# Kernel optimization log

Measured on AMD Instinct MI355X. Metric: run time of the kernel, lower is better.

The kernel has to match this reference:

```python
import jax, jax.numpy as jnp
import numpy as np

B, C, H, W = 2, 512, 48, 48
HEADS = 8          # head_dim = C // HEADS = 64
GROUPS = 32        # min(32, ceil(512/4)) = 32
EPS = 1e-5


def setup_inputs() -> dict:
    key = jax.random.key(0)
    ks = jax.random.split(key, 5)
    return {
        "x": jax.random.normal(ks[0], (B, C, H, W), jnp.float32),
        "gn_w": jnp.ones((C,), jnp.float32),
        "gn_b": jnp.zeros((C,), jnp.float32),
        # 1x1 convs stored as [out, in] matrices
        "qkv_w": jax.random.normal(ks[1], (3 * C, C), jnp.float32) / np.float32(np.sqrt(C)),
        "qkv_b": jax.random.normal(ks[2], (3 * C,), jnp.float32) * 0.01,
        "proj_w": jax.random.normal(ks[3], (C, C), jnp.float32) / np.float32(np.sqrt(C)),
        "proj_b": jax.random.normal(ks[4], (C,), jnp.float32) * 0.01,
    }


def _group_norm(x, w, b):
    b_, c_, h_, w_ = x.shape
    xg = x.reshape(b_, GROUPS, c_ // GROUPS, h_, w_)
    mean = xg.mean(axis=(2, 3, 4), keepdims=True)
    var = xg.var(axis=(2, 3, 4), keepdims=True)  # biased, matches F.group_norm
    xn = ((xg - mean) * jax.lax.rsqrt(var + EPS)).reshape(b_, c_, h_, w_)
    return xn * w[None, :, None, None] + b[None, :, None, None]


def reference(x, gn_w, gn_b, qkv_w, qkv_b, proj_w, proj_b):
    bx, cx, hx, wx = x.shape
    d = cx // HEADS
    n = hx * wx
    xn = _group_norm(x, gn_w, gn_b)
    # qkv 1x1 conv -> [B, 3C, H, W]
    y = jnp.einsum('oc,bchw->bohw', qkv_w, xn) + qkv_b[None, :, None, None]
    # torch: y.reshape(B*heads, d, 3, N).unbind(2)  (channel layout: head, chan, qkv)
    qkv = y.reshape(bx * HEADS, d, 3, n)
    q, k, v = qkv[:, :, 0, :], qkv[:, :, 1, :], qkv[:, :, 2, :]
    scale = np.float32(1.0 / np.sqrt(d))
    # AttentionOp: fp32 QK^T + softmax over keys (axis=2)
    w_attn = jax.nn.softmax(jnp.einsum('ncq,nck->nqk', q, k * scale), axis=2)
    a = jnp.einsum('nqk,nck->ncq', w_attn, v).reshape(bx, cx, hx, wx)
    out = jnp.einsum('oc,bchw->bohw', proj_w, a) + proj_b[None, :, None, None]
    return out + x
```

## Files before the change

kernel.cpp:

```cpp
#include <hip/hip_runtime.h>

typedef __bf16 bf16;
typedef __bf16 bf16x8 __attribute__((ext_vector_type(8)));
typedef __bf16 bf16x4 __attribute__((ext_vector_type(4)));
typedef float f32x4 __attribute__((ext_vector_type(4)));

#define B_ 2
#define C_ 512
#define HW_ 2304
#define GROUPS_ 32
#define CPG_ 16
#define EPS_ 1e-5f
#define THR_ 8.0f
#define LOG2E_ 1.44269504f
#define EXP2(x) __builtin_amdgcn_exp2f(x)

__device__ __forceinline__ void gload_lds16(const bf16* g, bf16* l) {
  __builtin_amdgcn_global_load_lds((const __attribute__((address_space(1))) void*)g,
                                   (__attribute__((address_space(3))) void*)l, 16, 0, 0);
}

__global__ __launch_bounds__(256) void pre_k(const float* __restrict__ x,
                                             const float* __restrict__ qkv_w,
                                             const float* __restrict__ qkv_b,
                                             const float* __restrict__ proj_w,
                                             float* __restrict__ ps,
                                             float* __restrict__ pss,
                                             bf16* __restrict__ wqkv,
                                             bf16* __restrict__ wp,
                                             float* __restrict__ bqkv) {
  int blk = blockIdx.x;
  if (blk < 512) {
    int bg = blk >> 3, seg = blk & 7;
    const int n4 = CPG_ * HW_ / 4 / 8;
    const float4* p = (const float4*)(x + (long)bg * CPG_ * HW_) + (long)seg * n4;
    float s = 0.f, ss = 0.f;
    for (int i = threadIdx.x; i < n4; i += 256) {
      float4 v = p[i];
      s += v.x + v.y + v.z + v.w;
      ss += v.x * v.x + v.y * v.y + v.z * v.z + v.w * v.w;
    }
#pragma unroll
    for (int d = 1; d < 64; d <<= 1) { s += __shfl_xor(s, d); ss += __shfl_xor(ss, d); }
    __shared__ float rs[4], rss[4];
    int wave = threadIdx.x >> 6, lane = threadIdx.x & 63;
    if (lane == 0) { rs[wave] = s; rss[wave] = ss; }
    __syncthreads();
    if (threadIdx.x == 0) {
      ps[blk] = rs[0] + rs[1] + rs[2] + rs[3];
      pss[blk] = rss[0] + rss[1] + rss[2] + rss[3];
    }
  } else {
    int idx = (blk - 512) * 256 + threadIdx.x;
    int r = idx >> 9, c = idx & 511;
    int src = (r < 512) ? 3 * r : (r < 1024 ? 3 * (r - 512) + 1 : 3 * (r - 1024) + 2);
    float sc = (r < 512) ? 0.125f * LOG2E_ : 1.0f;
    wqkv[idx] = (bf16)(qkv_w[(long)src * 512 + c] * sc);
    if (idx < 512 * 512) wp[idx] = (bf16)(proj_w[idx]);
    if (idx < 1536) {
      int sb = (idx < 512) ? 3 * idx : (idx < 1024 ? 3 * (idx - 512) + 1 : 3 * (idx - 1024) + 2);
      float sc2 = (idx < 512) ? 0.125f * LOG2E_ : 1.0f;
      bqkv[idx] = qkv_b[sb] * sc2;
    }
  }
}

__global__ __launch_bounds__(256) void gn_apply_k(const float* __restrict__ x,
                                                  const float* __restrict__ gw,
                                                  const float* __restrict__ gb,
                                                  const float* __restrict__ ps,
                                                  const float* __restrict__ pss,
                                                  bf16* __restrict__ xnT) {
  int n0 = blockIdx.x * 64, c0 = blockIdx.y * 32, b = blockIdx.z;
  int nn = n0 + (threadIdx.x & 63);
  int cb = c0 + ((threadIdx.x >> 6) << 3);
  int gi = b * GROUPS_ + (cb >> 4);
  float s = 0.f, ss = 0.f;
#pragma unroll
  for (int k = 0; k < 8; ++k) { s += ps[gi * 8 + k]; ss += pss[gi * 8 + k]; }
  const float invN = 1.0f / (float)(CPG_ * HW_);
  float mu = s * invN;
  float var = ss * invN - mu * mu;
  float rstd = rsqrtf(var + EPS_);
  bf16x8 o;
#pragma unroll
  for (int j = 0; j < 8; ++j) {
    int c = cb + j;
    float sc = rstd * gw[c];
    float sh = gb[c] - mu * sc;
    float v = x[((long)b * C_ + c) * HW_ + nn];
    o[j] = (bf16)(v * sc + sh);
  }
  *(bf16x8*)&xnT[((long)b * HW_ + nn) * C_ + cb] = o;
}

__global__ __launch_bounds__(256) void gemm_qkv_k(const bf16* __restrict__ A,
                                                  const bf16* __restrict__ BT,
                                                  const float* __restrict__ bias,
                                                  bf16* __restrict__ yT,
                                                  bf16* __restrict__ vOut) {
  constexpr int KK = 512;
  constexpr int NSTEP = KK >> 6;
  int b = blockIdx.z;
  A += (long)HW_ * 512 * b;
  yT += (long)HW_ * 1024 * b;
  vOut += (long)512 * HW_ * b;
  int m0 = blockIdx.y * 64, n0 = blockIdx.x * 64;
  int tid = threadIdx.x, lane = tid & 63, wave = tid >> 6;
  int wm = (wave >> 1) << 5, wn = (wave & 1) << 5;
  int fr = lane & 15, g = lane >> 4;
  __shared__ __align__(16) bf16 As[3][64 * 64];
  __shared__ __align__(16) bf16 Bs[3][64 * 64];
  int sr = tid >> 3;
  int swz = (((tid & 7) + sr) & 7) << 3;
  const bf16* gA = A + (long)(m0 + sr) * KK + swz;
  const bf16* gB = BT + (long)(n0 + sr) * KK + swz;
  int o0 = ((g - fr) & 7) << 3;
  int o1 = ((4 + g - fr) & 7) << 3;
  f32x4 acc[2][2] = {};
  gload_lds16(gA, &As[0][tid * 8]);
  gload_lds16(gA + 32 * KK, &As[0][2048 + tid * 8]);
  gload_lds16(gB, &Bs[0][tid * 8]);
  gload_lds16(gB + 32 * KK, &Bs[0][2048 + tid * 8]);
  gload_lds16(gA + 64, &As[1][tid * 8]);
  gload_lds16(gA + 32 * KK + 64, &As[1][2048 + tid * 8]);
  gload_lds16(gB + 64, &Bs[1][tid * 8]);
  gload_lds16(gB + 32 * KK + 64, &Bs[1][2048 + tid * 8]);
  asm volatile("s_waitcnt vmcnt(4)" ::: "memory");
  __builtin_amdgcn_s_barrier();
#pragma unroll
  for (int t = 0; t < NSTEP; ++t) {
    const int cur = t % 3;
    if (t + 2 < NSTEP) {
      const int nb = (t + 2) % 3;
      int k0 = (t + 2) << 6;
      gload_lds16(gA + k0, &As[nb][tid * 8]);
      gload_lds16(gA + 32 * KK + k0, &As[nb][2048 + tid * 8]);
      gload_lds16(gB + k0, &Bs[nb][tid * 8]);
      gload_lds16(gB + 32 * KK + k0, &Bs[nb][2048 + tid * 8]);
    }
    bf16x8 a00 = *(bf16x8*)&As[cur][(wm + fr) * 64 + o0];
    bf16x8 a01 = *(bf16x8*)&As[cur][(wm + fr) * 64 + o1];
    bf16x8 a10 = *(bf16x8*)&As[cur][(wm + 16 + fr) * 64 + o0];
    bf16x8 a11 = *(bf16x8*)&As[cur][(wm + 16 + fr) * 64 + o1];
    bf16x8 b00 = *(bf16x8*)&Bs[cur][(wn + fr) * 64 + o0];
    bf16x8 b01 = *(bf16x8*)&Bs[cur][(wn + fr) * 64 + o1];
    bf16x8 b10 = *(bf16x8*)&Bs[cur][(wn + 16 + fr) * 64 + o0];
    bf16x8 b11 = *(bf16x8*)&Bs[cur][(wn + 16 + fr) * 64 + o1];
    acc[0][0] = __builtin_amdgcn_mfma_f32_16x16x32_bf16(a00, b00, acc[0][0], 0, 0, 0);
    acc[0][0] = __builtin_amdgcn_mfma_f32_16x16x32_bf16(a01, b01, acc[0][0], 0, 0, 0);
    acc[0][1] = __builtin_amdgcn_mfma_f32_16x16x32_bf16(a00, b10, acc[0][1], 0, 0, 0);
    acc[0][1] = __builtin_amdgcn_mfma_f32_16x16x32_bf16(a01, b11, acc[0][1], 0, 0, 0);
    acc[1][0] = __builtin_amdgcn_mfma_f32_16x16x32_bf16(a10, b00, acc[1][0], 0, 0, 0);
    acc[1][0] = __builtin_amdgcn_mfma_f32_16x16x32_bf16(a11, b01, acc[1][0], 0, 0, 0);
    acc[1][1] = __builtin_amdgcn_mfma_f32_16x16x32_bf16(a10, b10, acc[1][1], 0, 0, 0);
    acc[1][1] = __builtin_amdgcn_mfma_f32_16x16x32_bf16(a11, b11, acc[1][1], 0, 0, 0);
    if (t + 2 < NSTEP) {
      asm volatile("s_waitcnt vmcnt(4) lgkmcnt(0)" ::: "memory");
    } else if (t + 1 < NSTEP) {
      asm volatile("s_waitcnt vmcnt(0) lgkmcnt(0)" ::: "memory");
    }
    if (t + 1 < NSTEP) __builtin_amdgcn_s_barrier();
  }
  int rbase = (lane >> 4) << 2;
  if (n0 < 1024) {
#pragma unroll
    for (int mi = 0; mi < 2; ++mi)
#pragma unroll
      for (int nj = 0; nj < 2; ++nj)
#pragma unroll
        for (int reg = 0; reg < 4; ++reg) {
          int row = m0 + wm + (mi << 4) + rbase + reg;
          int col = n0 + wn + (nj << 4) + fr;
          yT[(long)row * 1024 + col] = (bf16)(acc[mi][nj][reg] + bias[col]);
        }
  } else {
#pragma unroll
    for (int mi = 0; mi < 2; ++mi)
#pragma unroll
      for (int nj = 0; nj < 2; ++nj) {
        int row0 = m0 + wm + (mi << 4) + rbase;
        int ch = n0 - 1024 + wn + (nj << 4) + fr;
        float bs = bias[n0 + wn + (nj << 4) + fr];
        bf16x4 ov = {(bf16)(acc[mi][nj][0] + bs), (bf16)(acc[mi][nj][1] + bs),
                     (bf16)(acc[mi][nj][2] + bs), (bf16)(acc[mi][nj][3] + bs)};
        *(bf16x4*)&vOut[(long)ch * HW_ + row0] = ov;
      }
  }
}

template <int BIAS_MODE, bool RESID, typename OUT_T>
__global__ __launch_bounds__(256) void gemm_k(const bf16* __restrict__ A,
                                              const bf16* __restrict__ BT,
                                              const float* __restrict__ bias,
                                              const float* __restrict__ resid,
                                              OUT_T* __restrict__ Cc,
                                              int M, int N,
                                              long sA, long sBT, long sC) {
  constexpr int KK = 512;
  constexpr int NSTEP = KK >> 6;
  int b = blockIdx.z;
  A += sA * b;
  BT += sBT * b;
  Cc += sC * b;
  const float* R = RESID ? (resid + sC * b) : nullptr;
  int m0 = blockIdx.y * 64, n0 = blockIdx.x * 64;
  int tid = threadIdx.x, lane = tid & 63, wave = tid >> 6;
  int wm = (wave >> 1) << 5, wn = (wave & 1) << 5;
  int fr = lane & 15, g = lane >> 4;
  __shared__ __align__(16) bf16 As[3][64 * 64];
  __shared__ __align__(16) bf16 Bs[3][64 * 64];
  int sr = tid >> 3;
  int swz = (((tid & 7) + sr) & 7) << 3;
  const bf16* gA = A + (long)(m0 + sr) * KK + swz;
  const bf16* gB = BT + (long)(n0 + sr) * KK + swz;
  int o0 = ((g - fr) & 7) << 3;
  int o1 = ((4 + g - fr) & 7) << 3;
  f32x4 acc[2][2] = {};
  gload_lds16(gA, &As[0][tid * 8]);
  gload_lds16(gA + 32 * KK, &As[0][2048 + tid * 8]);
  gload_lds16(gB, &Bs[0][tid * 8]);
  gload_lds16(gB + 32 * KK, &Bs[0][2048 + tid * 8]);
  gload_lds16(gA + 64, &As[1][tid * 8]);
  gload_lds16(gA + 32 * KK + 64, &As[1][2048 + tid * 8]);
  gload_lds16(gB + 64, &Bs[1][tid * 8]);
  gload_lds16(gB + 32 * KK + 64, &Bs[1][2048 + tid * 8]);
  asm volatile("s_waitcnt vmcnt(4)" ::: "memory");
  __builtin_amdgcn_s_barrier();
#pragma unroll
  for (int t = 0; t < NSTEP; ++t) {
    const int cur = t % 3;
    if (t + 2 < NSTEP) {
      const int nb = (t + 2) % 3;
      int k0 = (t + 2) << 6;
      gload_lds16(gA + k0, &As[nb][tid * 8]);
      gload_lds16(gA + 32 * KK + k0, &As[nb][2048 + tid * 8]);
      gload_lds16(gB + k0, &Bs[nb][tid * 8]);
      gload_lds16(gB + 32 * KK + k0, &Bs[nb][2048 + tid * 8]);
    }
    bf16x8 a00 = *(bf16x8*)&As[cur][(wm + fr) * 64 + o0];
    bf16x8 a01 = *(bf16x8*)&As[cur][(wm + fr) * 64 + o1];
    bf16x8 a10 = *(bf16x8*)&As[cur][(wm + 16 + fr) * 64 + o0];
    bf16x8 a11 = *(bf16x8*)&As[cur][(wm + 16 + fr) * 64 + o1];
    bf16x8 b00 = *(bf16x8*)&Bs[cur][(wn + fr) * 64 + o0];
    bf16x8 b01 = *(bf16x8*)&Bs[cur][(wn + fr) * 64 + o1];
    bf16x8 b10 = *(bf16x8*)&Bs[cur][(wn + 16 + fr) * 64 + o0];
    bf16x8 b11 = *(bf16x8*)&Bs[cur][(wn + 16 + fr) * 64 + o1];
    acc[0][0] = __builtin_amdgcn_mfma_f32_16x16x32_bf16(a00, b00, acc[0][0], 0, 0, 0);
    acc[0][0] = __builtin_amdgcn_mfma_f32_16x16x32_bf16(a01, b01, acc[0][0], 0, 0, 0);
    acc[0][1] = __builtin_amdgcn_mfma_f32_16x16x32_bf16(a00, b10, acc[0][1], 0, 0, 0);
    acc[0][1] = __builtin_amdgcn_mfma_f32_16x16x32_bf16(a01, b11, acc[0][1], 0, 0, 0);
    acc[1][0] = __builtin_amdgcn_mfma_f32_16x16x32_bf16(a10, b00, acc[1][0], 0, 0, 0);
    acc[1][0] = __builtin_amdgcn_mfma_f32_16x16x32_bf16(a11, b01, acc[1][0], 0, 0, 0);
    acc[1][1] = __builtin_amdgcn_mfma_f32_16x16x32_bf16(a10, b10, acc[1][1], 0, 0, 0);
    acc[1][1] = __builtin_amdgcn_mfma_f32_16x16x32_bf16(a11, b11, acc[1][1], 0, 0, 0);
    if (t + 2 < NSTEP) {
      asm volatile("s_waitcnt vmcnt(4) lgkmcnt(0)" ::: "memory");
    } else if (t + 1 < NSTEP) {
      asm volatile("s_waitcnt vmcnt(0) lgkmcnt(0)" ::: "memory");
    }
    if (t + 1 < NSTEP) __builtin_amdgcn_s_barrier();
  }
  int rbase = (lane >> 4) << 2;
#pragma unroll
  for (int mi = 0; mi < 2; ++mi)
#pragma unroll
    for (int nj = 0; nj < 2; ++nj)
#pragma unroll
      for (int reg = 0; reg < 4; ++reg) {
        int row = m0 + wm + (mi << 4) + rbase + reg;
        int col = n0 + wn + (nj << 4) + fr;
        float v = acc[mi][nj][reg];
        if (BIAS_MODE == 1) v += bias[row];
        if (BIAS_MODE == 2) v += bias[col];
        if (RESID) v += R[(long)row * N + col];
        Cc[(long)row * N + col] = (OUT_T)v;
      }
}

template <int NS>
__global__ __launch_bounds__(512) void attn_k(const bf16* __restrict__ yT,
                                              const bf16* __restrict__ V,
                                              bf16* __restrict__ Op,
                                              float* __restrict__ Mp,
                                              float* __restrict__ Lp) {
  const int n = HW_;
  constexpr int NT = (HW_ / NS) / 64;
  int bh = blockIdx.y, b = bh >> 3, h = bh & 7;
  int split = blockIdx.z;
  int q0 = blockIdx.x * 128;
  int kbeg = split * (n / NS);
  int tid = threadIdx.x, lane = tid & 63, wave = tid >> 6;
  int fr = lane & 15, g = lane >> 4, kg = g << 3;
  const bf16* yTb = yT + (long)b * n * 1024;
  const bf16* Vb = V + ((long)b * C_ + h * 64) * n;
  const bf16* Kb = yTb + 512 + h * 64;

  int qrow = q0 + (wave << 4) + fr;
  const bf16* qp = yTb + (long)qrow * 1024 + h * 64;
  bf16x8 qf0 = *(const bf16x8*)(qp + kg);
  bf16x8 qf1 = *(const bf16x8*)(qp + 32 + kg);

  __shared__ __align__(16) bf16 Kt[2][64][64];
  __shared__ __align__(16) bf16 Vt[2][64][64];

  int o0 = ((g + fr) & 7) << 3;
  int o1 = ((4 + g + fr) & 7) << 3;

  float m_run = -1e30f, l_run = 0.f;
  f32x4 oacc[4] = {};

  int r0 = tid >> 3;
  int ck = tid & 7;
  int c0e = ck << 3;
  int pk = ((ck + r0) & 7) << 3;
  int vs = (c0e & 32) | ((c0e & 8) << 1) | ((c0e & 16) >> 2);
  int cv = vs >> 3, sub = vs & 7;
  int pv0 = (((cv + r0) & 7) << 3) + sub;
  int pv1 = (((cv + 1 + r0) & 7) << 3) + sub;

  const bf16* kptr = Kb + (long)(kbeg + r0) * 1024 + c0e;
  const bf16* vptr = Vb + (long)r0 * n + kbeg + c0e;
  uint4 rk = *(const uint4*)kptr;
  uint4 rv = *(const uint4*)vptr;
  *(uint4*)&Kt[0][r0][pk] = rk;
  *(uint2*)&Vt[0][r0][pv0] = make_uint2(rv.x, rv.y);
  *(uint2*)&Vt[0][r0][pv1] = make_uint2(rv.z, rv.w);
  kptr += 64 * 1024;
  vptr += 64;
  rk = *(const uint4*)kptr;
  rv = *(const uint4*)vptr;
  __syncthreads();

  for (int t = 0; t < NT; ++t) {
    int cur = t & 1;
    f32x4 s[4] = {};
    __builtin_amdgcn_s_setprio(1);
#pragma unroll
    for (int nj = 0; nj < 4; ++nj) {
      bf16x8 kf0 = *(bf16x8*)&Kt[cur][(nj << 4) + fr][o0];
      bf16x8 kf1 = *(bf16x8*)&Kt[cur][(nj << 4) + fr][o1];
      s[nj] = __builtin_amdgcn_mfma_f32_16x16x32_bf16(kf0, qf0, s[nj], 0, 0, 0);
      s[nj] = __builtin_amdgcn_mfma_f32_16x16x32_bf16(kf1, qf1, s[nj], 0, 0, 0);
    }
    __builtin_amdgcn_s_setprio(0);
    if (t + 1 < NT) {
      int nb = cur ^ 1;
      *(uint4*)&Kt[nb][r0][pk] = rk;
      *(uint2*)&Vt[nb][r0][pv0] = make_uint2(rv.x, rv.y);
      *(uint2*)&Vt[nb][r0][pv1] = make_uint2(rv.z, rv.w);
      if (t + 2 < NT) {
        kptr += 64 * 1024;
        vptr += 64;
        rk = *(const uint4*)kptr;
        rv = *(const uint4*)vptr;
      }
    }
    float pm = fmaxf(fmaxf(s[0][0], s[0][1]), fmaxf(s[0][2], s[0][3]));
#pragma unroll
    for (int nj = 1; nj < 4; ++nj)
      pm = fmaxf(pm, fmaxf(fmaxf(s[nj][0], s[nj][1]), fmaxf(s[nj][2], s[nj][3])));
    pm = fmaxf(pm, __shfl_xor(pm, 16));
    pm = fmaxf(pm, __shfl_xor(pm, 32));
    if (__any(pm > m_run + THR_)) {
      float mn = fmaxf(m_run, pm);
      float corr = EXP2(m_run - mn);
      m_run = mn;
      l_run *= corr;
#pragma unroll
      for (int dj = 0; dj < 4; ++dj)
#pragma unroll
        for (int r = 0; r < 4; ++r) oacc[dj][r] *= corr;
    }
    float ls = 0.f;
    bf16x8 pa0, pa1;
#pragma unroll
    for (int r = 0; r < 4; ++r) {
      float p0 = EXP2(s[0][r] - m_run);
      float p1 = EXP2(s[1][r] - m_run);
      float p2 = EXP2(s[2][r] - m_run);
      float p3 = EXP2(s[3][r] - m_run);
      ls += (p0 + p1) + (p2 + p3);
      pa0[r] = (bf16)p0;
      pa0[4 + r] = (bf16)p1;
      pa1[r] = (bf16)p2;
      pa1[4 + r] = (bf16)p3;
    }
    ls += __shfl_xor(ls, 16);
    ls += __shfl_xor(ls, 32);
    l_run += ls;
    __builtin_amdgcn_s_setprio(1);
#pragma unroll
    for (int dj = 0; dj < 4; ++dj) {
      bf16x8 vf0 = *(bf16x8*)&Vt[cur][(dj << 4) + fr][o0];
      bf16x8 vf1 = *(bf16x8*)&Vt[cur][(dj << 4) + fr][o1];
      oacc[dj] = __builtin_amdgcn_mfma_f32_16x16x32_bf16(vf0, pa0, oacc[dj], 0, 0, 0);
      oacc[dj] = __builtin_amdgcn_mfma_f32_16x16x32_bf16(vf1, pa1, oacc[dj], 0, 0, 0);
    }
    __builtin_amdgcn_s_setprio(0);
    __syncthreads();
  }
  long orow = (long)(split * 16 + bh) * n + q0 + (wave << 4) + fr;
#pragma unroll
  for (int dj = 0; dj < 4; ++dj) {
    bf16x4 ov = {(bf16)oacc[dj][0], (bf16)oacc[dj][1], (bf16)oacc[dj][2], (bf16)oacc[dj][3]};
    *(bf16x4*)&Op[orow * 64 + (dj << 4) + (g << 2)] = ov;
  }
  if (g == 0) {
    Mp[orow] = m_run;
    Lp[orow] = l_run;
  }
}

template <int NS>
__global__ __launch_bounds__(256) void attn_merge_k(const bf16* __restrict__ Op,
                                                    const float* __restrict__ Mp,
                                                    const float* __restrict__ Lp,
                                                    bf16* __restrict__ aT) {
  int bh = blockIdx.y, b = bh >> 3, h = bh & 7;
  int gi = blockIdx.x * 256 + threadIdx.x;
  int nrow = gi >> 3, dd8 = (gi & 7) << 3;
  long idx[NS];
  float mm = -1e30f;
#pragma unroll
  for (int s = 0; s < NS; ++s) {
    idx[s] = (long)(s * 16 + bh) * HW_ + nrow;
    mm = fmaxf(mm, Mp[idx[s]]);
  }
  float l = 0.f, w[NS];
#pragma unroll
  for (int s = 0; s < NS; ++s) {
    w[s] = EXP2(Mp[idx[s]] - mm);
    l += Lp[idx[s]] * w[s];
  }
  float invl = 1.f / l;
  float oaccf[8] = {};
#pragma unroll
  for (int s = 0; s < NS; ++s) {
    bf16x8 o = *(const bf16x8*)&Op[idx[s] * 64 + dd8];
    float ws = w[s] * invl;
#pragma unroll
    for (int j = 0; j < 8; ++j) oaccf[j] += (float)o[j] * ws;
  }
  bf16x8 o;
#pragma unroll
  for (int j = 0; j < 8; ++j) o[j] = (bf16)oaccf[j];
  *(bf16x8*)&aT[((long)b * HW_ + nrow) * C_ + h * 64 + dd8] = o;
}

extern "C" void kernel_launch(void* const* d_in, const int* in_sizes, int n_in,
                              void* d_out, int out_size, void* d_ws, size_t ws_size,
                              hipStream_t stream) {
  const float* x = (const float*)d_in[0];
  const float* gn_w = (const float*)d_in[1];
  const float* gn_b = (const float*)d_in[2];
  const float* qkv_w = (const float*)d_in[3];
  const float* qkv_b = (const float*)d_in[4];
  const float* proj_w = (const float*)d_in[5];
  const float* proj_b = (const float*)d_in[6];
  float* out = (float*)d_out;

  char* ws = (char*)d_ws;
  float* ps = (float*)ws;    ws += 2048;
  float* pss = (float*)ws;   ws += 2048;
  float* bqkv = (float*)ws;  ws += 6144;
  bf16* wqkv = (bf16*)ws;    ws += 1536l * 512 * 2;
  bf16* wp = (bf16*)ws;      ws += 512l * 512 * 2;
  bf16* xnT = (bf16*)ws;     ws += 2l * HW_ * 512 * 2;
  bf16* yT = (bf16*)ws;      ws += 2l * HW_ * 1024 * 2;
  bf16* v = (bf16*)ws;       ws += 2l * 512 * HW_ * 2;
  bf16* aT = (bf16*)ws;      ws += 2l * HW_ * 512 * 2;
  bf16* Op = (bf16*)ws;
  size_t base_used = (size_t)(ws - (char*)d_ws);
  size_t need4 = base_used + 4ull * 16 * HW_ * 64 * 2 + 2ull * 4 * 16 * HW_ * 4;
  int NS = (ws_size >= need4) ? 4 : 2;
  ws += (size_t)NS * 16 * HW_ * 64 * 2;
  float* Mp = (float*)ws;    ws += (size_t)NS * 16 * HW_ * 4;
  float* Lp = (float*)ws;    ws += (size_t)NS * 16 * HW_ * 4;

  pre_k<<<3584, 256, 0, stream>>>(x, qkv_w, qkv_b, proj_w, ps, pss, wqkv, wp, bqkv);
  gn_apply_k<<<dim3(36, 16, 2), 256, 0, stream>>>(x, gn_w, gn_b, ps, pss, xnT);
  gemm_qkv_k<<<dim3(24, 36, 2), 256, 0, stream>>>(xnT, wqkv, bqkv, yT, v);
  if (NS == 4) {
    attn_k<4><<<dim3(18, 16, 4), 512, 0, stream>>>(yT, v, Op, Mp, Lp);
    attn_merge_k<4><<<dim3(72, 16), 256, 0, stream>>>(Op, Mp, Lp, aT);
  } else {
    attn_k<2><<<dim3(18, 16, 2), 512, 0, stream>>>(yT, v, Op, Mp, Lp);
    attn_merge_k<2><<<dim3(72, 16), 256, 0, stream>>>(Op, Mp, Lp, aT);
  }
  gemm_k<1, true, float><<<dim3(36, 8, 2), 256, 0, stream>>>(
      wp, aT, proj_b, x, out, 512, 2304, 0, (long)HW_ * 512, 512l * HW_);
}
```

Measured before the change: 85.49 us.

## Fuse split-K attention merge into projection GEMM B-operand load

The separate attention merge kernel, which combined partial softmax outputs into aT, is removed. The projection GEMM now reads the partial outputs plus their max and sum stats, merges them in registers for each K-step, and writes the merged bf16 tile into LDS as the B operand. This drops one launch and the aT round trip through global memory. The cost is that every M-tile block (8 per column) recomputes the merge and rereads the partials, and each step now waits on vmcnt(0) with register-staged loads instead of asynchronous LDS loads. Separately, the group-norm apply kernel computes mean and rstd once per group in shared memory instead of in every thread.

New measurement: 91.60 us. 1.07x slower.

```diff
diff --git a/kernel.cpp b/kernel.cpp
--- a/kernel.cpp
+++ b/kernel.cpp
@@ -74,14 +74,21 @@
   int n0 = blockIdx.x * 64, c0 = blockIdx.y * 32, b = blockIdx.z;
   int nn = n0 + (threadIdx.x & 63);
   int cb = c0 + ((threadIdx.x >> 6) << 3);
-  int gi = b * GROUPS_ + (cb >> 4);
-  float s = 0.f, ss = 0.f;
-#pragma unroll
-  for (int k = 0; k < 8; ++k) { s += ps[gi * 8 + k]; ss += pss[gi * 8 + k]; }
-  const float invN = 1.0f / (float)(CPG_ * HW_);
-  float mu = s * invN;
-  float var = ss * invN - mu * mu;
-  float rstd = rsqrtf(var + EPS_);
+  __shared__ float smu[2], srstd[2];
+  if (threadIdx.x < 2) {
+    int gi = b * GROUPS_ + (c0 >> 4) + threadIdx.x;
+    float s = 0.f, ss = 0.f;
+#pragma unroll
+    for (int k = 0; k < 8; ++k) { s += ps[gi * 8 + k]; ss += pss[gi * 8 + k]; }
+    const float invN = 1.0f / (float)(CPG_ * HW_);
+    float mu = s * invN;
+    float var = ss * invN - mu * mu;
+    smu[threadIdx.x] = mu;
+    srstd[threadIdx.x] = rsqrtf(var + EPS_);
+  }
+  __syncthreads();
+  int gsel = threadIdx.x >> 7;
+  float mu = smu[gsel], rstd = srstd[gsel];
   bf16x8 o;
 #pragma unroll
   for (int j = 0; j < 8; ++j) {
@@ -189,95 +196,6 @@
   }
 }
 
-template <int BIAS_MODE, bool RESID, typename OUT_T>
-__global__ __launch_bounds__(256) void gemm_k(const bf16* __restrict__ A,
-                                              const bf16* __restrict__ BT,
-                                              const float* __restrict__ bias,
-                                              const float* __restrict__ resid,
-                                              OUT_T* __restrict__ Cc,
-                                              int M, int N,
-                                              long sA, long sBT, long sC) {
-  constexpr int KK = 512;
-  constexpr int NSTEP = KK >> 6;
-  int b = blockIdx.z;
-  A += sA * b;
-  BT += sBT * b;
-  Cc += sC * b;
-  const float* R = RESID ? (resid + sC * b) : nullptr;
-  int m0 = blockIdx.y * 64, n0 = blockIdx.x * 64;
-  int tid = threadIdx.x, lane = tid & 63, wave = tid >> 6;
-  int wm = (wave >> 1) << 5, wn = (wave & 1) << 5;
-  int fr = lane & 15, g = lane >> 4;
-  __shared__ __align__(16) bf16 As[3][64 * 64];
-  __shared__ __align__(16) bf16 Bs[3][64 * 64];
-  int sr = tid >> 3;
-  int swz = (((tid & 7) + sr) & 7) << 3;
-  const bf16* gA = A + (long)(m0 + sr) * KK + swz;
-  const bf16* gB = BT + (long)(n0 + sr) * KK + swz;
-  int o0 = ((g - fr) & 7) << 3;
-  int o1 = ((4 + g - fr) & 7) << 3;
-  f32x4 acc[2][2] = {};
-  gload_lds16(gA, &As[0][tid * 8]);
-  gload_lds16(gA + 32 * KK, &As[0][2048 + tid * 8]);
-  gload_lds16(gB, &Bs[0][tid * 8]);
-  gload_lds16(gB + 32 * KK, &Bs[0][2048 + tid * 8]);
-  gload_lds16(gA + 64, &As[1][tid * 8]);
-  gload_lds16(gA + 32 * KK + 64, &As[1][2048 + tid * 8]);
-  gload_lds16(gB + 64, &Bs[1][tid * 8]);
-  gload_lds16(gB + 32 * KK + 64, &Bs[1][2048 + tid * 8]);
-  asm volatile("s_waitcnt vmcnt(4)" ::: "memory");
-  __builtin_amdgcn_s_barrier();
-#pragma unroll
-  for (int t = 0; t < NSTEP; ++t) {
-    const int cur = t % 3;
-    if (t + 2 < NSTEP) {
-      const int nb = (t + 2) % 3;
-      int k0 = (t + 2) << 6;
-      gload_lds16(gA + k0, &As[nb][tid * 8]);
-      gload_lds16(gA + 32 * KK + k0, &As[nb][2048 + tid * 8]);
-      gload_lds16(gB + k0, &Bs[nb][tid * 8]);
-      gload_lds16(gB + 32 * KK + k0, &Bs[nb][2048 + tid * 8]);
-    }
-    bf16x8 a00 = *(bf16x8*)&As[cur][(wm + fr) * 64 + o0];
-    bf16x8 a01 = *(bf16x8*)&As[cur][(wm + fr) * 64 + o1];
-    bf16x8 a10 = *(bf16x8*)&As[cur][(wm + 16 + fr) * 64 + o0];
-    bf16x8 a11 = *(bf16x8*)&As[cur][(wm + 16 + fr) * 64 + o1];
-    bf16x8 b00 = *(bf16x8*)&Bs[cur][(wn + fr) * 64 + o0];
-    bf16x8 b01 = *(bf16x8*)&Bs[cur][(wn + fr) * 64 + o1];
-    bf16x8 b10 = *(bf16x8*)&Bs[cur][(wn + 16 + fr) * 64 + o0];
-    bf16x8 b11 = *(bf16x8*)&Bs[cur][(wn + 16 + fr) * 64 + o1];
-    acc[0][0] = __builtin_amdgcn_mfma_f32_16x16x32_bf16(a00, b00, acc[0][0], 0, 0, 0);
-    acc[0][0] = __builtin_amdgcn_mfma_f32_16x16x32_bf16(a01, b01, acc[0][0], 0, 0, 0);
-    acc[0][1] = __builtin_amdgcn_mfma_f32_16x16x32_bf16(a00, b10, acc[0][1], 0, 0, 0);
-    acc[0][1] = __builtin_amdgcn_mfma_f32_16x16x32_bf16(a01, b11, acc[0][1], 0, 0, 0);
-    acc[1][0] = __builtin_amdgcn_mfma_f32_16x16x32_bf16(a10, b00, acc[1][0], 0, 0, 0);
-    acc[1][0] = __builtin_amdgcn_mfma_f32_16x16x32_bf16(a11, b01, acc[1][0], 0, 0, 0);
-    acc[1][1] = __builtin_amdgcn_mfma_f32_16x16x32_bf16(a10, b10, acc[1][1], 0, 0, 0);
-    acc[1][1] = __builtin_amdgcn_mfma_f32_16x16x32_bf16(a11, b11, acc[1][1], 0, 0, 0);
-    if (t + 2 < NSTEP) {
-      asm volatile("s_waitcnt vmcnt(4) lgkmcnt(0)" ::: "memory");
-    } else if (t + 1 < NSTEP) {
-      asm volatile("s_waitcnt vmcnt(0) lgkmcnt(0)" ::: "memory");
-    }
-    if (t + 1 < NSTEP) __builtin_amdgcn_s_barrier();
-  }
-  int rbase = (lane >> 4) << 2;
-#pragma unroll
-  for (int mi = 0; mi < 2; ++mi)
-#pragma unroll
-    for (int nj = 0; nj < 2; ++nj)
-#pragma unroll
-      for (int reg = 0; reg < 4; ++reg) {
-        int row = m0 + wm + (mi << 4) + rbase + reg;
-        int col = n0 + wn + (nj << 4) + fr;
-        float v = acc[mi][nj][reg];
-        if (BIAS_MODE == 1) v += bias[row];
-        if (BIAS_MODE == 2) v += bias[col];
-        if (RESID) v += R[(long)row * N + col];
-        Cc[(long)row * N + col] = (OUT_T)v;
-      }
-}
-
 template <int NS>
 __global__ __launch_bounds__(512) void attn_k(const bf16* __restrict__ yT,
                                               const bf16* __restrict__ V,
@@ -413,39 +331,126 @@
 }
 
 template <int NS>
-__global__ __launch_bounds__(256) void attn_merge_k(const bf16* __restrict__ Op,
-                                                    const float* __restrict__ Mp,
-                                                    const float* __restrict__ Lp,
-                                                    bf16* __restrict__ aT) {
-  int bh = blockIdx.y, b = bh >> 3, h = bh & 7;
-  int gi = blockIdx.x * 256 + threadIdx.x;
-  int nrow = gi >> 3, dd8 = (gi & 7) << 3;
-  long idx[NS];
-  float mm = -1e30f;
-#pragma unroll
-  for (int s = 0; s < NS; ++s) {
-    idx[s] = (long)(s * 16 + bh) * HW_ + nrow;
-    mm = fmaxf(mm, Mp[idx[s]]);
-  }
-  float l = 0.f, w[NS];
-#pragma unroll
-  for (int s = 0; s < NS; ++s) {
-    w[s] = EXP2(Mp[idx[s]] - mm);
-    l += Lp[idx[s]] * w[s];
-  }
-  float invl = 1.f / l;
-  float oaccf[8] = {};
-#pragma unroll
-  for (int s = 0; s < NS; ++s) {
-    bf16x8 o = *(const bf16x8*)&Op[idx[s] * 64 + dd8];
-    float ws = w[s] * invl;
-#pragma unroll
-    for (int j = 0; j < 8; ++j) oaccf[j] += (float)o[j] * ws;
-  }
-  bf16x8 o;
-#pragma unroll
-  for (int j = 0; j < 8; ++j) o[j] = (bf16)oaccf[j];
-  *(bf16x8*)&aT[((long)b * HW_ + nrow) * C_ + h * 64 + dd8] = o;
+__global__ __launch_bounds__(256) void gemm_proj_k(const bf16* __restrict__ wp,
+                                                   const float* __restrict__ bias,
+                                                   const float* __restrict__ x,
+                                                   const bf16* __restrict__ Op,
+                                                   const float* __restrict__ Mp,
+                                                   const float* __restrict__ Lp,
+                                                   float* __restrict__ out) {
+  constexpr int KK = 512;
+  constexpr int NSTEP = 8;
+  int b = blockIdx.z;
+  const float* xb = x + (long)512 * HW_ * b;
+  float* outb = out + (long)512 * HW_ * b;
+  int m0 = blockIdx.y * 64, n0 = blockIdx.x * 64;
+  int tid = threadIdx.x, lane = tid & 63, wave = tid >> 6;
+  int wm = (wave >> 1) << 5, wn = (wave & 1) << 5;
+  int fr = lane & 15, g = lane >> 4;
+  __shared__ __align__(16) bf16 As[3][64 * 64];
+  __shared__ __align__(16) bf16 Bs[3][64 * 64];
+  int sr = tid >> 3;
+  int swz = (((tid & 7) + sr) & 7) << 3;
+  const bf16* gA = wp + (long)(m0 + sr) * KK + swz;
+  int lc = ((tid & 7) + sr) & 7;
+  int row0 = n0 + sr, row1 = n0 + sr + 32;
+  int o0 = ((g - fr) & 7) << 3;
+  int o1 = ((4 + g - fr) & 7) << 3;
+  f32x4 acc[2][2] = {};
+
+  bf16x8 opv[2][NS];
+  float mpv[2][NS], lpv[2][NS];
+
+#define LOADB(t)                                                              \
+  {                                                                           \
+    int bh = b * 8 + (t);                                                     \
+    _Pragma("unroll") for (int rr = 0; rr < 2; ++rr) {                        \
+      int rown = rr ? row1 : row0;                                            \
+      _Pragma("unroll") for (int s = 0; s < NS; ++s) {                        \
+        long ix = (long)(s * 16 + bh) * HW_ + rown;                           \
+        mpv[rr][s] = Mp[ix];                                                  \
+        lpv[rr][s] = Lp[ix];                                                  \
+        opv[rr][s] = *(const bf16x8*)&Op[ix * 64 + lc * 8];                   \
+      }                                                                       \
+    }                                                                         \
+  }
+
+#define WRITEB(buf)                                                           \
+  {                                                                           \
+    _Pragma("unroll") for (int rr = 0; rr < 2; ++rr) {                        \
+      float mm = mpv[rr][0];                                                  \
+      _Pragma("unroll") for (int s = 1; s < NS; ++s) mm = fmaxf(mm, mpv[rr][s]); \
+      float l = 0.f, wv[NS];                                                  \
+      _Pragma("unroll") for (int s = 0; s < NS; ++s) {                        \
+        wv[s] = EXP2(mpv[rr][s] - mm);                                        \
+        l += wv[s] * lpv[rr][s];                                              \
+      }                                                                       \
+      float invl = 1.f / l;                                                   \
+      float a8[8] = {};                                                       \
+      _Pragma("unroll") for (int s = 0; s < NS; ++s) {                        \
+        float wsc = wv[s] * invl;                                             \
+        _Pragma("unroll") for (int j = 0; j < 8; ++j)                         \
+            a8[j] += (float)opv[rr][s][j] * wsc;                              \
+      }                                                                       \
+      bf16x8 pk;                                                              \
+      _Pragma("unroll") for (int j = 0; j < 8; ++j) pk[j] = (bf16)a8[j];      \
+      *(bf16x8*)&Bs[buf][(rr ? 2048 : 0) + tid * 8] = pk;                     \
+    }                                                                         \
+  }
+
+  LOADB(0);
+  WRITEB(0);
+  gload_lds16(gA, &As[0][tid * 8]);
+  gload_lds16(gA + 32 * KK, &As[0][2048 + tid * 8]);
+  gload_lds16(gA + 64, &As[1][tid * 8]);
+  gload_lds16(gA + 32 * KK + 64, &As[1][2048 + tid * 8]);
+  asm volatile("s_waitcnt vmcnt(2) lgkmcnt(0)" ::: "memory");
+  __builtin_amdgcn_s_barrier();
+#pragma unroll
+  for (int t = 0; t < NSTEP; ++t) {
+    const int cur = t % 3;
+    if (t + 2 < NSTEP) {
+      int k0 = (t + 2) << 6;
+      gload_lds16(gA + k0, &As[(t + 2) % 3][tid * 8]);
+      gload_lds16(gA + 32 * KK + k0, &As[(t + 2) % 3][2048 + tid * 8]);
+    }
+    if (t + 1 < NSTEP) LOADB(t + 1);
+    bf16x8 a00 = *(bf16x8*)&As[cur][(wm + fr) * 64 + o0];
+    bf16x8 a01 = *(bf16x8*)&As[cur][(wm + fr) * 64 + o1];
+    bf16x8 a10 = *(bf16x8*)&As[cur][(wm + 16 + fr) * 64 + o0];
+    bf16x8 a11 = *(bf16x8*)&As[cur][(wm + 16 + fr) * 64 + o1];
+    bf16x8 b00 = *(bf16x8*)&Bs[cur][(wn + fr) * 64 + o0];
+    bf16x8 b01 = *(bf16x8*)&Bs[cur][(wn + fr) * 64 + o1];
+    bf16x8 b10 = *(bf16x8*)&Bs[cur][(wn + 16 + fr) * 64 + o0];
+    bf16x8 b11 = *(bf16x8*)&Bs[cur][(wn + 16 + fr) * 64 + o1];
+    acc[0][0] = __builtin_amdgcn_mfma_f32_16x16x32_bf16(a00, b00, acc[0][0], 0, 0, 0);
+    acc[0][0] = __builtin_amdgcn_mfma_f32_16x16x32_bf16(a01, b01, acc[0][0], 0, 0, 0);
+    acc[0][1] = __builtin_amdgcn_mfma_f32_16x16x32_bf16(a00, b10, acc[0][1], 0, 0, 0);
+    acc[0][1] = __builtin_amdgcn_mfma_f32_16x16x32_bf16(a01, b11, acc[0][1], 0, 0, 0);
+    acc[1][0] = __builtin_amdgcn_mfma_f32_16x16x32_bf16(a10, b00, acc[1][0], 0, 0, 0);
+    acc[1][0] = __builtin_amdgcn_mfma_f32_16x16x32_bf16(a11, b01, acc[1][0], 0, 0, 0);
+    acc[1][1] = __builtin_amdgcn_mfma_f32_16x16x32_bf16(a10, b10, acc[1][1], 0, 0, 0);
+    acc[1][1] = __builtin_amdgcn_mfma_f32_16x16x32_bf16(a11, b11, acc[1][1], 0, 0, 0);
+    if (t + 1 < NSTEP) {
+      WRITEB((t + 1) % 3);
+      asm volatile("s_waitcnt vmcnt(0) lgkmcnt(0)" ::: "memory");
+      __builtin_amdgcn_s_barrier();
+    }
+  }
+#undef LOADB
+#undef WRITEB
+  int rbase = (lane >> 4) << 2;
+#pragma unroll
+  for (int mi = 0; mi < 2; ++mi)
+#pragma unroll
+    for (int nj = 0; nj < 2; ++nj)
+#pragma unroll
+      for (int reg = 0; reg < 4; ++reg) {
+        int row = m0 + wm + (mi << 4) + rbase + reg;
+        int col = n0 + wn + (nj << 4) + fr;
+        float v = acc[mi][nj][reg] + bias[row] + xb[(long)row * HW_ + col];
+        outb[(long)row * HW_ + col] = v;
+      }
 }
 
 extern "C" void kernel_launch(void* const* d_in, const int* in_sizes, int n_in,
@@ -469,7 +474,6 @@
   bf16* xnT = (bf16*)ws;     ws += 2l * HW_ * 512 * 2;
   bf16* yT = (bf16*)ws;      ws += 2l * HW_ * 1024 * 2;
   bf16* v = (bf16*)ws;       ws += 2l * 512 * HW_ * 2;
-  bf16* aT = (bf16*)ws;      ws += 2l * HW_ * 512 * 2;
   bf16* Op = (bf16*)ws;
   size_t base_used = (size_t)(ws - (char*)d_ws);
   size_t need4 = base_used + 4ull * 16 * HW_ * 64 * 2 + 2ull * 4 * 16 * HW_ * 4;
@@ -483,11 +487,9 @@
   gemm_qkv_k<<<dim3(24, 36, 2), 256, 0, stream>>>(xnT, wqkv, bqkv, yT, v);
   if (NS == 4) {
     attn_k<4><<<dim3(18, 16, 4), 512, 0, stream>>>(yT, v, Op, Mp, Lp);
-    attn_merge_k<4><<<dim3(72, 16), 256, 0, stream>>>(Op, Mp, Lp, aT);
+    gemm_proj_k<4><<<dim3(36, 8, 2), 256, 0, stream>>>(wp, proj_b, x, Op, Mp, Lp, out);
   } else {
     attn_k<2><<<dim3(18, 16, 2), 512, 0, stream>>>(yT, v, Op, Mp, Lp);
-    attn_merge_k<2><<<dim3(72, 16), 256, 0, stream>>>(Op, Mp, Lp, aT);
-  }
-  gemm_k<1, true, float><<<dim3(36, 8, 2), 256, 0, stream>>>(
-      wp, aT, proj_b, x, out, 512, 2304, 0, (long)HW_ * 512, 512l * HW_);
-}
+    gemm_proj_k<2><<<dim3(36, 8, 2), 256, 0, stream>>>(wp, proj_b, x, Op, Mp, Lp, out);
+  }
+}
```
